# Performance work log

Measured on AMD Instinct MI355X. Metric: run time of the kernel, lower is better.

## Reference

```python
import jax, jax.numpy as jnp
import numpy as np

N_NODES = 20000
N_EDGES = 320000
N_FEAT = 128
MLP_HID = 64
N_GRAPHS = 16
N_LAYERS = 5
EPS = 1e-5


def setup_inputs() -> dict:
    key = jax.random.key(0)
    ks = jax.random.split(key, 8)
    x = jax.random.normal(ks[0], (N_NODES, N_FEAT), dtype=jnp.float32)
    edge_index = jax.random.randint(ks[1], (2, N_EDGES), 0, N_NODES, dtype=jnp.int64)
    batch = jnp.sort(jax.random.randint(ks[2], (N_NODES,), 0, N_GRAPHS, dtype=jnp.int64))
    W1 = jax.random.normal(ks[3], (N_LAYERS, N_FEAT, MLP_HID), dtype=jnp.float32) * 0.05
    b1 = jnp.zeros((N_LAYERS, MLP_HID), dtype=jnp.float32)
    W2 = jax.random.normal(ks[4], (N_LAYERS, MLP_HID, N_FEAT), dtype=jnp.float32) * 0.05
    b2 = jnp.zeros((N_LAYERS, N_FEAT), dtype=jnp.float32)
    gn_weight = jnp.ones((N_LAYERS, N_FEAT), dtype=jnp.float32)
    gn_bias = jnp.zeros((N_LAYERS, N_FEAT), dtype=jnp.float32)
    gn_scale = jnp.ones((N_LAYERS, N_FEAT), dtype=jnp.float32)
    lin_w = jax.random.normal(ks[5], (N_FEAT, 1), dtype=jnp.float32) * 0.05
    lin_b = jnp.zeros((1,), dtype=jnp.float32)
    return {"x": x, "edge_index": edge_index, "batch": batch,
            "W1": W1, "b1": b1, "W2": W2, "b2": b2,
            "gn_weight": gn_weight, "gn_bias": gn_bias, "gn_scale": gn_scale,
            "lin_w": lin_w, "lin_b": lin_b}


def _conv(h, src, dst, W1, b1, W2, b2):
    # message MLP is per-source-node, so compute MLP(x) once per node,
    # then gather by src and scatter-add to dst. Self loops add m[i] at i.
    m = jax.nn.relu(h @ W1 + b1) @ W2 + b2  # [N, C]
    return jax.ops.segment_sum(m[src], dst, num_segments=N_NODES) + m


def _graph_norm(h, batch, cnt, w, b, a):
    mean = jax.ops.segment_sum(h, batch, num_segments=N_GRAPHS) / cnt  # [G, C]
    out = h - a * mean[batch]
    var = jax.ops.segment_sum(out * out, batch, num_segments=N_GRAPHS) / cnt
    out = out * jax.lax.rsqrt(var[batch] + EPS)
    return w * out + b


def reference(x, edge_index, batch, W1, b1, W2, b2, gn_weight, gn_bias, gn_scale, lin_w, lin_b):
    src, dst = edge_index[0], edge_index[1]
    cnt = jax.ops.segment_sum(jnp.ones((N_NODES, 1), x.dtype), batch,
                              num_segments=N_GRAPHS)
    cnt = jnp.maximum(cnt, 1.0)  # [G, 1]
    h = x
    for i in range(N_LAYERS):
        g = _conv(h, src, dst, W1[i], b1[i], W2[i], b2[i])
        g = _graph_norm(g, batch, cnt, gn_weight[i], gn_bias[i], gn_scale[i])
        g = jax.nn.relu(g)  # dropout is identity in eval mode
        h = g if i == 0 else g + h  # residual from layer 2 onward
    pooled = jax.ops.segment_sum(h, batch, num_segments=N_GRAPHS) / cnt  # [G, C]
    return pooled @ lin_w + lin_b  # [G, 1]
```

## Files before the change

### kernel.cpp

```cpp
#include <hip/hip_runtime.h>

#define N_NODES 20000
#define N_EDGES 320000
#define N_FEAT 128
#define MLP_HID 64
#define N_GRAPHS 16
#define N_LAYERS 5
#define EPS 1e-5f

typedef __attribute__((ext_vector_type(8))) short short8;
typedef __attribute__((ext_vector_type(4))) float f32x4;

__device__ inline float bf2f(unsigned short u) { return __uint_as_float(((unsigned)u) << 16); }
__device__ inline unsigned short f2bf(float f) {
  unsigned u = __float_as_uint(f);
  u += 0x7FFF + ((u >> 16) & 1);
  return (unsigned short)(u >> 16);
}

__device__ __forceinline__ float apply1(float gvx, float hvx, float smx, float sex,
                                        float invc, float ac, float wx, float bx) {
  float mean = smx * invc;
  float ex2 = sex * invc;
  float var = fmaxf(ex2 - mean * mean * (2.0f * ac - ac * ac), 0.0f);
  float d = gvx - ac * mean;
  float y = wx * (d * rsqrtf(var + EPS)) + bx;
  y = fmaxf(y, 0.0f);
  return y + hvx;
}


__global__ __launch_bounds__(256) void k_deg(const int* __restrict__ dst, int* __restrict__ deg) {
  int e = blockIdx.x * 256 + threadIdx.x;
  atomicAdd(&deg[dst[e]], 1);
}

__global__ __launch_bounds__(1024) void k_scan(const int* __restrict__ deg, int* __restrict__ rowptr,
                                               int* __restrict__ cursor, const int* __restrict__ batch,
                                               float* __restrict__ cntf, float* __restrict__ pooled,
                                               float* __restrict__ s1, float* __restrict__ s2) {
  __shared__ int sdata[1024];
  __shared__ int spos[17];
  constexpr int CH = 20;
  int t = threadIdx.x;
  for (int i = t; i < N_GRAPHS * N_FEAT; i += 1024) pooled[i] = 0.0f;
  for (int i = t; i < N_LAYERS * N_GRAPHS * N_FEAT; i += 1024) { s1[i] = 0.0f; s2[i] = 0.0f; }
  int base = t * CH;
  int loc[CH];
  int partial = 0;
#pragma unroll
  for (int i = 0; i < CH; i++) {
    int idx = base + i;
    int v = (idx < N_NODES) ? deg[idx] : 0;
    loc[i] = v;
    partial += v;
  }
  sdata[t] = partial;
  __syncthreads();
  for (int off = 1; off < 1024; off <<= 1) {
    int v = (t >= off) ? sdata[t - off] : 0;
    __syncthreads();
    sdata[t] += v;
    __syncthreads();
  }
  int run = sdata[t] - partial;
#pragma unroll
  for (int i = 0; i < CH; i++) {
    int idx = base + i;
    if (idx < N_NODES) {
      rowptr[idx] = run;
      cursor[idx] = run;
      run += loc[i];
    }
  }
  if (t == 1023) rowptr[N_NODES] = sdata[1023];
  if (t < 17) {
    int lo = 0, hi = N_NODES;
    while (lo < hi) {
      int mid = (lo + hi) >> 1;
      if (batch[mid] < t) lo = mid + 1; else hi = mid;
    }
    spos[t] = lo;
  }
  __syncthreads();
  if (t < N_GRAPHS) cntf[t] = fmaxf((float)(spos[t + 1] - spos[t]), 1.0f);
}

__global__ __launch_bounds__(256) void k_fill(const int* __restrict__ src, const int* __restrict__ dst,
                                              int* __restrict__ cursor, int* __restrict__ src_sorted) {
  int e = blockIdx.x * 256 + threadIdx.x;
  int d = dst[e];
  int p = atomicAdd(&cursor[d], 1);
  src_sorted[p] = src[e];
}


__global__ __launch_bounds__(256) void k_prep(const float* __restrict__ W1, const float* __restrict__ W2,
                                              unsigned short* __restrict__ w1t, unsigned short* __restrict__ w2t,
                                              int* __restrict__ deg) {
  int idx = blockIdx.x * 256 + threadIdx.x;
  if (idx < N_NODES) deg[idx] = 0;
  if (idx < 40960) {
    int l = idx >> 13, rem = idx & 8191;
    int n = rem >> 7, k = rem & 127;
    w1t[idx] = f2bf(W1[l * 8192 + k * 64 + n]);
  } else {
    int j = idx - 40960;
    int l = j >> 13, rem = j & 8191;
    int n = rem >> 6, k = rem & 63;
    w2t[j] = f2bf(W2[l * 8192 + k * 128 + n]);
  }
}


#define PADK 136
#define PADH 72

__global__ __launch_bounds__(256) void k_mlp(const float* __restrict__ hin, unsigned short* __restrict__ mout,
                                             const unsigned short* __restrict__ w1t,
                                             const unsigned short* __restrict__ w2t,
                                             const float* __restrict__ b1, const float* __restrict__ b2) {
  __shared__ __align__(16) short hS[64 * PADK];
  __shared__ __align__(16) short w1S[64 * PADK];
  __shared__ __align__(16) short hidS[64 * PADH];
  __shared__ __align__(16) short w2S[128 * PADH];
  __shared__ float b1S[64];
  __shared__ float b2S[128];
  int t = threadIdx.x;
  int r0 = blockIdx.x * 64;
#pragma unroll
  for (int i = 0; i < 8; i++) {
    int idx = t + i * 256;
    int row = idx >> 5, c4 = idx & 31;
    float4 v = (r0 + row < N_NODES) ? ((const float4*)hin)[(size_t)(r0 + row) * 32 + c4]
                                    : make_float4(0.f, 0.f, 0.f, 0.f);
    ushort4 s;
    s.x = f2bf(v.x); s.y = f2bf(v.y); s.z = f2bf(v.z); s.w = f2bf(v.w);
    *(ushort4*)&hS[row * PADK + c4 * 4] = s;
  }
#pragma unroll
  for (int i = 0; i < 4; i++) {
    int idx = t + i * 256;
    *(int4*)&w1S[(idx >> 4) * PADK + (idx & 15) * 8] = ((const int4*)w1t)[idx];
    *(int4*)&w2S[(idx >> 3) * PADH + (idx & 7) * 8] = ((const int4*)w2t)[idx];
  }
  if (t < 64) b1S[t] = b1[t];
  else if (t < 192) b2S[t - 64] = b2[t - 64];
  __syncthreads();

  int w = t >> 6, lane = t & 63, lm = lane & 15, quad = lane >> 4;
  int mrow = w * 16 + lm;
  int orow = w * 16 + quad * 4;

  f32x4 zero = {0.f, 0.f, 0.f, 0.f};
  f32x4 acc[4] = {zero, zero, zero, zero};
#pragma unroll
  for (int k0 = 0; k0 < 128; k0 += 32) {
    short8 a = *(const short8*)&hS[mrow * PADK + k0 + quad * 8];
#pragma unroll
    for (int nt = 0; nt < 4; nt++) {
      short8 b = *(const short8*)&w1S[(nt * 16 + lm) * PADK + k0 + quad * 8];
      acc[nt] = __builtin_amdgcn_mfma_f32_16x16x32_bf16(a, b, acc[nt], 0, 0, 0);
    }
  }
#pragma unroll
  for (int nt = 0; nt < 4; nt++) {
    int col = nt * 16 + lm;
    float bb = b1S[col];
#pragma unroll
    for (int r = 0; r < 4; r++)
      hidS[(orow + r) * PADH + col] = (short)f2bf(fmaxf(acc[nt][r] + bb, 0.0f));
  }
  __syncthreads();

  f32x4 acc2[8] = {zero, zero, zero, zero, zero, zero, zero, zero};
#pragma unroll
  for (int k0 = 0; k0 < 64; k0 += 32) {
    short8 a = *(const short8*)&hidS[mrow * PADH + k0 + quad * 8];
#pragma unroll
    for (int nt = 0; nt < 8; nt++) {
      short8 b = *(const short8*)&w2S[(nt * 16 + lm) * PADH + k0 + quad * 8];
      acc2[nt] = __builtin_amdgcn_mfma_f32_16x16x32_bf16(a, b, acc2[nt], 0, 0, 0);
    }
  }
#pragma unroll
  for (int nt = 0; nt < 8; nt++) {
    int col = nt * 16 + lm;
    float bb = b2S[col];
#pragma unroll
    for (int r = 0; r < 4; r++)
      hS[(orow + r) * PADK + col] = (short)f2bf(acc2[nt][r] + bb);
  }
  __syncthreads();
#pragma unroll
  for (int i = 0; i < 4; i++) {
    int idx = t + i * 256;
    int row = idx >> 4, cc = idx & 15;
    if (r0 + row < N_NODES)
      ((int4*)mout)[(size_t)(r0 + row) * 16 + cc] = *(const int4*)&hS[row * PADK + cc * 8];
  }
}


__global__ __launch_bounds__(256) void k_scatter(const unsigned short* __restrict__ mbf, float* __restrict__ g,
                                                 const int* __restrict__ rowptr, const int* __restrict__ srcs,
                                                 const int* __restrict__ batch,
                                                 float* __restrict__ s1, float* __restrict__ s2) {
  __shared__ float sS1[4][128];
  __shared__ float sS2[4][128];
  int t = threadIdx.x;
  int node = (blockIdx.x * 256 + t) >> 6;
  int w = t >> 6;
  int lane = t & 63;
  int quarter = lane >> 4;
  int q16 = lane & 15;
  const float4* m4 = (const float4*)mbf;
  float acc[8];
  union BU { float4 f; unsigned short u[8]; };
  if (quarter == 0) {
    BU U; U.f = m4[(size_t)node * 16 + q16];
#pragma unroll
    for (int j = 0; j < 8; j++) acc[j] = bf2f(U.u[j]);
  } else {
#pragma unroll
    for (int j = 0; j < 8; j++) acc[j] = 0.0f;
  }
  int e = rowptr[node], e1 = rowptr[node + 1];
  for (; e + 16 <= e1; e += 16) {
    int i0 = srcs[e + quarter];
    int i1 = srcs[e + 4 + quarter];
    int i2 = srcs[e + 8 + quarter];
    int i3 = srcs[e + 12 + quarter];
    BU U0, U1, U2, U3;
    U0.f = m4[(size_t)i0 * 16 + q16];
    U1.f = m4[(size_t)i1 * 16 + q16];
    U2.f = m4[(size_t)i2 * 16 + q16];
    U3.f = m4[(size_t)i3 * 16 + q16];
#pragma unroll
    for (int j = 0; j < 8; j++)
      acc[j] += (bf2f(U0.u[j]) + bf2f(U1.u[j])) + (bf2f(U2.u[j]) + bf2f(U3.u[j]));
  }
  for (; e + 4 <= e1; e += 4) {
    BU U0; U0.f = m4[(size_t)srcs[e + quarter] * 16 + q16];
#pragma unroll
    for (int j = 0; j < 8; j++) acc[j] += bf2f(U0.u[j]);
  }
  if (e + quarter < e1) {
    BU U0; U0.f = m4[(size_t)srcs[e + quarter] * 16 + q16];
#pragma unroll
    for (int j = 0; j < 8; j++) acc[j] += bf2f(U0.u[j]);
  }
#pragma unroll
  for (int j = 0; j < 8; j++) {
    acc[j] += __shfl_xor(acc[j], 16);
    acc[j] += __shfl_xor(acc[j], 32);
  }
  if (quarter == 0) {
    float4* g4 = (float4*)(g + (size_t)node * 128 + q16 * 8);
    g4[0] = make_float4(acc[0], acc[1], acc[2], acc[3]);
    g4[1] = make_float4(acc[4], acc[5], acc[6], acc[7]);
#pragma unroll
    for (int j = 0; j < 8; j++) {
      float v = acc[j];
      sS1[w][q16 * 8 + j] = v;
      sS2[w][q16 * 8 + j] = v * v;
    }
  }
  __syncthreads();
  int n0 = blockIdx.x * 4;
  int gA = batch[n0], gB = batch[n0 + 3];
  if (t < 128) {
    if (gA == gB) {
      atomicAdd(&s1[gA * 128 + t], sS1[0][t] + sS1[1][t] + sS1[2][t] + sS1[3][t]);
    } else {
#pragma unroll
      for (int ww = 0; ww < 4; ww++) atomicAdd(&s1[batch[n0 + ww] * 128 + t], sS1[ww][t]);
    }
  } else {
    int c = t - 128;
    if (gA == gB) {
      atomicAdd(&s2[gA * 128 + c], sS2[0][c] + sS2[1][c] + sS2[2][c] + sS2[3][c]);
    } else {
#pragma unroll
      for (int ww = 0; ww < 4; ww++) atomicAdd(&s2[batch[n0 + ww] * 128 + c], sS2[ww][c]);
    }
  }
}


__global__ __launch_bounds__(256) void k_apply(const float* __restrict__ gin, float* __restrict__ h,
                                               const int* __restrict__ batch,
                                               const float* __restrict__ s1, const float* __restrict__ s2,
                                               const float* __restrict__ cntf,
                                               const float* __restrict__ w, const float* __restrict__ b,
                                               const float* __restrict__ a, int residual) {
  int idx = blockIdx.x * 256 + threadIdx.x;
  int n = idx >> 5, c4 = idx & 31;
  int gg = batch[n];
  float invc = 1.0f / cntf[gg];
  float4 sm = ((const float4*)s1)[gg * 32 + c4];
  float4 se = ((const float4*)s2)[gg * 32 + c4];
  float4 av = ((const float4*)a)[c4];
  float4 wv = ((const float4*)w)[c4];
  float4 bv = ((const float4*)b)[c4];
  float4 gv = ((const float4*)gin)[idx];
  float4 hv = make_float4(0.f, 0.f, 0.f, 0.f);
  if (residual) hv = ((const float4*)h)[idx];
  float4 o;
  o.x = apply1(gv.x, hv.x, sm.x, se.x, invc, av.x, wv.x, bv.x);
  o.y = apply1(gv.y, hv.y, sm.y, se.y, invc, av.y, wv.y, bv.y);
  o.z = apply1(gv.z, hv.z, sm.z, se.z, invc, av.z, wv.z, bv.z);
  o.w = apply1(gv.w, hv.w, sm.w, se.w, invc, av.w, wv.w, bv.w);
  ((float4*)h)[idx] = o;
}


__global__ __launch_bounds__(256) void k_apply_pool(const float* __restrict__ gin, const float* __restrict__ h,
                                                    const int* __restrict__ batch,
                                                    const float* __restrict__ s1, const float* __restrict__ s2,
                                                    const float* __restrict__ cntf,
                                                    const float* __restrict__ gw, const float* __restrict__ gb,
                                                    const float* __restrict__ ga,
                                                    float* __restrict__ pooled) {
  __shared__ float pS[8][128];
  int t = threadIdx.x;
  int idx = blockIdx.x * 256 + t;
  int n = idx >> 5, c4 = idx & 31;
  int gg = batch[n];
  float invc = 1.0f / cntf[gg];
  float4 sm = ((const float4*)s1)[gg * 32 + c4];
  float4 se = ((const float4*)s2)[gg * 32 + c4];
  float4 av = ((const float4*)ga)[c4];
  float4 wv = ((const float4*)gw)[c4];
  float4 bv = ((const float4*)gb)[c4];
  float4 gv = ((const float4*)gin)[idx];
  float4 hv = ((const float4*)h)[idx];
  float4 o;
  o.x = apply1(gv.x, hv.x, sm.x, se.x, invc, av.x, wv.x, bv.x);
  o.y = apply1(gv.y, hv.y, sm.y, se.y, invc, av.y, wv.y, bv.y);
  o.z = apply1(gv.z, hv.z, sm.z, se.z, invc, av.z, wv.z, bv.z);
  o.w = apply1(gv.w, hv.w, sm.w, se.w, invc, av.w, wv.w, bv.w);
  *(float4*)&pS[t >> 5][c4 * 4] = o;
  __syncthreads();
  int n0 = blockIdx.x * 8;
  int gA = batch[n0], gB = batch[n0 + 7];
  if (t < 128) {
    if (gA == gB) {
      float s = 0.f;
#pragma unroll
      for (int ww = 0; ww < 8; ww++) s += pS[ww][t];
      atomicAdd(&pooled[gA * 128 + t], s);
    } else {
#pragma unroll
      for (int ww = 0; ww < 8; ww++) atomicAdd(&pooled[batch[n0 + ww] * 128 + t], pS[ww][t]);
    }
  }
}


__global__ __launch_bounds__(256) void k_final(const float* __restrict__ pooled, const float* __restrict__ cntf,
                                               const float* __restrict__ lw, const float* __restrict__ lb,
                                               float* __restrict__ out) {
  int lane = threadIdx.x & 63, wave = threadIdx.x >> 6;
  for (int gi = 0; gi < 4; gi++) {
    int gidx = wave * 4 + gi;
    float s = pooled[gidx * 128 + lane] * lw[lane] + pooled[gidx * 128 + 64 + lane] * lw[64 + lane];
    for (int o = 32; o >= 1; o >>= 1) s += __shfl_down(s, o);
    if (lane == 0) out[gidx] = s / cntf[gidx] + lb[0];
  }
}


extern "C" void kernel_launch(void* const* d_in, const int* in_sizes, int n_in,
                              void* d_out, int out_size, void* d_ws, size_t ws_size,
                              hipStream_t stream) {
  const float* x = (const float*)d_in[0];
  const int* ei = (const int*)d_in[1];
  const int* batch = (const int*)d_in[2];
  const float* W1 = (const float*)d_in[3];
  const float* b1 = (const float*)d_in[4];
  const float* W2 = (const float*)d_in[5];
  const float* b2 = (const float*)d_in[6];
  const float* gnw = (const float*)d_in[7];
  const float* gnb = (const float*)d_in[8];
  const float* gna = (const float*)d_in[9];
  const float* lw = (const float*)d_in[10];
  const float* lb = (const float*)d_in[11];
  float* out = (float*)d_out;

  const int* srcI = ei;
  const int* dstI = ei + N_EDGES;

  char* p = (char*)d_ws;
  float* hbuf = (float*)(p + 0);
  unsigned short* mbuf = (unsigned short*)(p + 10240000);
  float* gbuf = (float*)(p + 15360000);
  int* src_sorted = (int*)(p + 25600000);
  int* rowptr = (int*)(p + 26880000);
  int* cursor = (int*)(p + 26960128);
  int* deg = (int*)(p + 27040128);
  float* cntf = (float*)(p + 27120128);
  float* s1buf = (float*)(p + 27120192);
  float* s2buf = (float*)(p + 27161152);
  float* pooled = (float*)(p + 27202112);
  unsigned short* w1t = (unsigned short*)(p + 27210304);
  unsigned short* w2t = (unsigned short*)(p + 27292224);

  k_prep<<<320, 256, 0, stream>>>(W1, W2, w1t, w2t, deg);
  k_deg<<<N_EDGES / 256, 256, 0, stream>>>(dstI, deg);
  k_scan<<<1, 1024, 0, stream>>>(deg, rowptr, cursor, batch, cntf, pooled, s1buf, s2buf);
  k_fill<<<N_EDGES / 256, 256, 0, stream>>>(srcI, dstI, cursor, src_sorted);

  const float* hin = x;
  for (int i = 0; i < N_LAYERS; i++) {
    k_mlp<<<(N_NODES + 63) / 64, 256, 0, stream>>>(hin, mbuf, w1t + (size_t)i * 8192, w2t + (size_t)i * 8192,
                                                   b1 + (size_t)i * 64, b2 + (size_t)i * 128);
    k_scatter<<<N_NODES / 4, 256, 0, stream>>>(mbuf, gbuf, rowptr, src_sorted, batch,
                                               s1buf + (size_t)i * 2048, s2buf + (size_t)i * 2048);
    if (i < N_LAYERS - 1) {
      k_apply<<<N_NODES * N_FEAT / 4 / 256, 256, 0, stream>>>(
          gbuf, hbuf, batch, s1buf + (size_t)i * 2048, s2buf + (size_t)i * 2048, cntf,
          gnw + (size_t)i * 128, gnb + (size_t)i * 128, gna + (size_t)i * 128, i > 0 ? 1 : 0);
      hin = hbuf;
    } else {
      k_apply_pool<<<N_NODES / 8, 256, 0, stream>>>(
          gbuf, hbuf, batch, s1buf + (size_t)i * 2048, s2buf + (size_t)i * 2048, cntf,
          gnw + (size_t)i * 128, gnb + (size_t)i * 128, gna + (size_t)i * 128, pooled);
    }
  }

  k_final<<<1, 256, 0, stream>>>(pooled, cntf, lw, lb, out);
}
```

Measured before the change: 389.8 us.

## Split scatter gather into column passes and move group stats to a separate kernel

The CSR gather kernel now runs four column passes, each launching a grid of blocks over all nodes. Each wave covers a 32-column slice of one node, with 16 lanes spread across edges and 4 lanes across columns. The aim is to shrink the working set of the gathered bf16 message rows per pass so they reuse better in cache, and to spread edges over more lanes. The per-graph sum and sum-of-squares reduction, with its shared-memory staging and atomics, moves out of the scatter into a new k_stats kernel that rereads the fp32 output. This costs an extra launch, an extra read of the full output and four times the rowptr/src index reads.

Measured after the change: 416.7 us. +6.9%, slower.

```diff
diff --git a/kernel.cpp b/kernel.cpp
--- a/kernel.cpp
+++ b/kernel.cpp
@@ -202,89 +202,76 @@
 }
 
 
+#define NCHUNK 5000
+
 __global__ __launch_bounds__(256) void k_scatter(const unsigned short* __restrict__ mbf, float* __restrict__ g,
-                                                 const int* __restrict__ rowptr, const int* __restrict__ srcs,
-                                                 const int* __restrict__ batch,
-                                                 float* __restrict__ s1, float* __restrict__ s2) {
-  __shared__ float sS1[4][128];
-  __shared__ float sS2[4][128];
+                                                 const int* __restrict__ rowptr, const int* __restrict__ srcs) {
+  int bidx = blockIdx.x;
+  int pass = bidx / NCHUNK;
+  int chunk = bidx - pass * NCHUNK;
   int t = threadIdx.x;
-  int node = (blockIdx.x * 256 + t) >> 6;
   int w = t >> 6;
+  int node = chunk * 4 + w;
   int lane = t & 63;
-  int quarter = lane >> 4;
-  int q16 = lane & 15;
+  int egrp = lane >> 2;
+  int cofs = lane & 3;
   const float4* m4 = (const float4*)mbf;
+  int mcol = pass * 4 + cofs;
   float acc[8];
   union BU { float4 f; unsigned short u[8]; };
-  if (quarter == 0) {
-    BU U; U.f = m4[(size_t)node * 16 + q16];
+  if (egrp == 0) {
+    BU U; U.f = m4[(size_t)node * 16 + mcol];
 #pragma unroll
     for (int j = 0; j < 8; j++) acc[j] = bf2f(U.u[j]);
   } else {
 #pragma unroll
     for (int j = 0; j < 8; j++) acc[j] = 0.0f;
   }
-  int e = rowptr[node], e1 = rowptr[node + 1];
-  for (; e + 16 <= e1; e += 16) {
-    int i0 = srcs[e + quarter];
-    int i1 = srcs[e + 4 + quarter];
-    int i2 = srcs[e + 8 + quarter];
-    int i3 = srcs[e + 12 + quarter];
-    BU U0, U1, U2, U3;
-    U0.f = m4[(size_t)i0 * 16 + q16];
-    U1.f = m4[(size_t)i1 * 16 + q16];
-    U2.f = m4[(size_t)i2 * 16 + q16];
-    U3.f = m4[(size_t)i3 * 16 + q16];
-#pragma unroll
-    for (int j = 0; j < 8; j++)
-      acc[j] += (bf2f(U0.u[j]) + bf2f(U1.u[j])) + (bf2f(U2.u[j]) + bf2f(U3.u[j]));
-  }
-  for (; e + 4 <= e1; e += 4) {
-    BU U0; U0.f = m4[(size_t)srcs[e + quarter] * 16 + q16];
-#pragma unroll
-    for (int j = 0; j < 8; j++) acc[j] += bf2f(U0.u[j]);
-  }
-  if (e + quarter < e1) {
-    BU U0; U0.f = m4[(size_t)srcs[e + quarter] * 16 + q16];
-#pragma unroll
-    for (int j = 0; j < 8; j++) acc[j] += bf2f(U0.u[j]);
+  int e1 = rowptr[node + 1];
+  for (int e = rowptr[node] + egrp; e < e1; e += 16) {
+    BU U; U.f = m4[(size_t)srcs[e] * 16 + mcol];
+#pragma unroll
+    for (int j = 0; j < 8; j++) acc[j] += bf2f(U.u[j]);
   }
 #pragma unroll
   for (int j = 0; j < 8; j++) {
+    acc[j] += __shfl_xor(acc[j], 4);
+    acc[j] += __shfl_xor(acc[j], 8);
     acc[j] += __shfl_xor(acc[j], 16);
     acc[j] += __shfl_xor(acc[j], 32);
   }
-  if (quarter == 0) {
-    float4* g4 = (float4*)(g + (size_t)node * 128 + q16 * 8);
+  if (egrp == 0) {
+    float4* g4 = (float4*)(g + (size_t)node * 128 + pass * 32 + cofs * 8);
     g4[0] = make_float4(acc[0], acc[1], acc[2], acc[3]);
     g4[1] = make_float4(acc[4], acc[5], acc[6], acc[7]);
-#pragma unroll
-    for (int j = 0; j < 8; j++) {
-      float v = acc[j];
-      sS1[w][q16 * 8 + j] = v;
-      sS2[w][q16 * 8 + j] = v * v;
-    }
-  }
-  __syncthreads();
-  int n0 = blockIdx.x * 4;
-  int gA = batch[n0], gB = batch[n0 + 3];
-  if (t < 128) {
-    if (gA == gB) {
-      atomicAdd(&s1[gA * 128 + t], sS1[0][t] + sS1[1][t] + sS1[2][t] + sS1[3][t]);
-    } else {
-#pragma unroll
-      for (int ww = 0; ww < 4; ww++) atomicAdd(&s1[batch[n0 + ww] * 128 + t], sS1[ww][t]);
-    }
-  } else {
-    int c = t - 128;
-    if (gA == gB) {
-      atomicAdd(&s2[gA * 128 + c], sS2[0][c] + sS2[1][c] + sS2[2][c] + sS2[3][c]);
-    } else {
-#pragma unroll
-      for (int ww = 0; ww < 4; ww++) atomicAdd(&s2[batch[n0 + ww] * 128 + c], sS2[ww][c]);
-    }
-  }
+  }
+}
+
+
+#define STAT_CHUNK 8
+
+__global__ __launch_bounds__(128) void k_stats(const float* __restrict__ in, const int* __restrict__ batch,
+                                               float* __restrict__ s1, float* __restrict__ s2) {
+  int n0 = blockIdx.x * STAT_CHUNK;
+  int c = threadIdx.x;
+  int curg = batch[n0];
+  float a1 = 0.0f, a2 = 0.0f;
+#pragma unroll
+  for (int k = 0; k < STAT_CHUNK; k++) {
+    int n = n0 + k;
+    int gg = batch[n];
+    if (gg != curg) {
+      atomicAdd(&s1[curg * 128 + c], a1);
+      atomicAdd(&s2[curg * 128 + c], a2);
+      a1 = 0.0f; a2 = 0.0f;
+      curg = gg;
+    }
+    float v = in[(size_t)n * 128 + c];
+    a1 += v;
+    a2 += v * v;
+  }
+  atomicAdd(&s1[curg * 128 + c], a1);
+  atomicAdd(&s2[curg * 128 + c], a2);
 }
 
 
@@ -415,8 +402,9 @@
   for (int i = 0; i < N_LAYERS; i++) {
     k_mlp<<<(N_NODES + 63) / 64, 256, 0, stream>>>(hin, mbuf, w1t + (size_t)i * 8192, w2t + (size_t)i * 8192,
                                                    b1 + (size_t)i * 64, b2 + (size_t)i * 128);
-    k_scatter<<<N_NODES / 4, 256, 0, stream>>>(mbuf, gbuf, rowptr, src_sorted, batch,
-                                               s1buf + (size_t)i * 2048, s2buf + (size_t)i * 2048);
+    k_scatter<<<4 * NCHUNK, 256, 0, stream>>>(mbuf, gbuf, rowptr, src_sorted);
+    k_stats<<<N_NODES / STAT_CHUNK, 128, 0, stream>>>(gbuf, batch,
+                                                      s1buf + (size_t)i * 2048, s2buf + (size_t)i * 2048);
     if (i < N_LAYERS - 1) {
       k_apply<<<N_NODES * N_FEAT / 4 / 256, 256, 0, stream>>>(
           gbuf, hbuf, batch, s1buf + (size_t)i * 2048, s2buf + (size_t)i * 2048, cntf,
```
